# Kernel tuning notes

Measured on AMD Instinct MI355X. Metric: run time of the kernel, lower is better.

Reference implementation:

```python
import jax, jax.numpy as jnp
import numpy as np

N = 100000      # nodes
E = 3200000     # edges
NG = 64         # graphs in batch
F_IN, H1, H2 = 128, 128, 64
DENSE = 16 * 8  # first_dense_neurons * second_dense_neurons
LABELS = 2


def setup_inputs() -> dict:
    key = jax.random.key(0)
    ks = jax.random.split(key, 12)
    x = jax.random.normal(ks[0], (N, F_IN), dtype=jnp.float32)
    edge_index = jax.random.randint(ks[1], (2, E), 0, N, dtype=jnp.int32)
    batch = jnp.sort(jax.random.randint(ks[2], (N,), 0, NG, dtype=jnp.int32))
    s = 0.05
    W1 = jax.random.normal(ks[3], (F_IN, H1), dtype=jnp.float32) * s
    b1 = jnp.zeros((H1,), dtype=jnp.float32)
    W2 = jax.random.normal(ks[4], (H1, H2), dtype=jnp.float32) * s
    b2 = jnp.zeros((H2,), dtype=jnp.float32)
    Wf1 = jax.random.normal(ks[5], (H2, DENSE), dtype=jnp.float32) * s
    bf1 = jnp.zeros((DENSE,), dtype=jnp.float32)
    Wf2 = jax.random.normal(ks[6], (DENSE, LABELS), dtype=jnp.float32) * s
    bf2 = jnp.zeros((LABELS,), dtype=jnp.float32)
    return {"x": x, "W1": W1, "b1": b1, "W2": W2, "b2": b2,
            "Wf1": Wf1, "bf1": bf1, "Wf2": Wf2, "bf2": bf2,
            "edge_index": edge_index, "batch": batch}


def _gcn_conv(x, W, b, src, dst, dis):
    # PyG GCNConv: h = x @ W, propagate with sym norm (self-loops included)
    h = x @ W
    coef = (dis[src] * dis[dst])[:, None]          # [E,1]
    agg = jax.ops.segment_sum(h[src] * coef, dst, num_segments=N)
    agg = agg + h * (dis * dis)[:, None]           # self-loop term
    return agg + b


def reference(x, W1, b1, W2, b2, Wf1, bf1, Wf2, bf2, edge_index, batch):
    src, dst = edge_index[0], edge_index[1]
    # degree with self-loops, symmetric normalization D^-1/2 (A+I) D^-1/2
    deg = 1.0 + jax.ops.segment_sum(jnp.ones((E,), x.dtype), dst, num_segments=N)
    dis = jax.lax.rsqrt(deg)
    h1 = jax.nn.relu(_gcn_conv(x, W1, b1, src, dst, dis))
    h2 = jax.nn.relu(_gcn_conv(h1, W2, b2, src, dst, dis))
    a1 = h2 @ Wf1 + bf1                            # [N, DENSE] (dropout: eval mode)
    counts = jax.ops.segment_sum(jnp.ones((N,), x.dtype), batch, num_segments=NG)
    graph_embedding = jax.ops.segment_sum(a1, batch, num_segments=NG) / jnp.maximum(counts, 1.0)[:, None]
    ic_predictions = graph_embedding @ Wf2 + bf2   # [NG, LABELS]
    penalty = jnp.float32(0.0)
    return (graph_embedding, penalty, ic_predictions)
```

## Files before the change

### kernel.cpp

```cpp
#include <hip/hip_runtime.h>


typedef __attribute__((ext_vector_type(8))) short bfrag;
typedef __attribute__((ext_vector_type(16))) float f32x16;
typedef __attribute__((ext_vector_type(2))) float floatx2;

__device__ __forceinline__ unsigned short f2bf(float f) {
    unsigned int u = __builtin_bit_cast(unsigned int, f);
    u = (u + 0x7FFFu + ((u >> 16) & 1u)) >> 16;
    return (unsigned short)u;
}
__device__ __forceinline__ float bf2f(unsigned int lo16) {
    unsigned int v = lo16 << 16;
    return __builtin_bit_cast(float, v);
}
__device__ __forceinline__ unsigned char f2fp8(float f) {
    return (unsigned char)(__builtin_amdgcn_cvt_pk_fp8_f32(f, f, 0, false) & 0xFF);
}
__device__ __forceinline__ void macc8f8(float* acc, const uint2& v, float c) {
    floatx2 f0 = __builtin_amdgcn_cvt_pk_f32_fp8((int)v.x, false);
    floatx2 f1 = __builtin_amdgcn_cvt_pk_f32_fp8((int)v.x, true);
    floatx2 f2 = __builtin_amdgcn_cvt_pk_f32_fp8((int)v.y, false);
    floatx2 f3 = __builtin_amdgcn_cvt_pk_f32_fp8((int)v.y, true);
    acc[0] += f0.x * c; acc[1] += f0.y * c;
    acc[2] += f1.x * c; acc[3] += f1.y * c;
    acc[4] += f2.x * c; acc[5] += f2.y * c;
    acc[6] += f3.x * c; acc[7] += f3.y * c;
}

template <int K, int NC>
__device__ __forceinline__ void wprep_body(int bid, const float* __restrict__ W,
                                           unsigned short* __restrict__ Wf) {
    constexpr int CT = NC / 32, KT = K / 16;
    int idx = bid * 256 + threadIdx.x;
    if (idx >= KT * CT * 64) return;
    int l = idx & 63;
    int fi = idx >> 6;
    int ct = fi % CT, kt = fi / CT;
    int n = ct * 32 + (l & 31);
    int k0 = kt * 16 + 8 * (l >> 5);
    unsigned short v[8];
#pragma unroll
    for (int j = 0; j < 8; ++j) v[j] = f2bf(W[(size_t)(k0 + j) * NC + n]);
    uint4 o;
    o.x = (unsigned)v[0] | ((unsigned)v[1] << 16);
    o.y = (unsigned)v[2] | ((unsigned)v[3] << 16);
    o.z = (unsigned)v[4] | ((unsigned)v[5] << 16);
    o.w = (unsigned)v[6] | ((unsigned)v[7] << 16);
    *(uint4*)&Wf[(size_t)idx * 8] = o;
}

__global__ __launch_bounds__(256) void fusedA_kernel(const int* __restrict__ dst,
                                                     int* __restrict__ bcount, int E, int EB,
                                                     const float* __restrict__ W1,
                                                     unsigned short* __restrict__ Wp1,
                                                     const float* __restrict__ W2,
                                                     unsigned short* __restrict__ Wp2) {
    __shared__ int h[256];
    int b = blockIdx.x;
    int t = threadIdx.x;
    if (b < EB) {
        h[t] = 0;
        __syncthreads();
        int base = b * 4096;
#pragma unroll
        for (int i = 0; i < 16; ++i) {
            int e = base + t + i * 256;
            if (e < E) atomicAdd(&h[dst[e] >> 9], 1);
        }
        __syncthreads();
        if (h[t] > 0) atomicAdd(&bcount[t], h[t]);
    } else if (b < EB + 8) {
        wprep_body<128, 128>(b - EB, W1, Wp1);
    } else {
        wprep_body<128, 64>(b - EB - 8, W2, Wp2);
    }
}

__global__ __launch_bounds__(256) void bucket_scatter_kernel(const int* __restrict__ src,
                                                             const int* __restrict__ dst,
                                                             const int* __restrict__ bcount,
                                                             int* __restrict__ bfill,
                                                             unsigned int* __restrict__ stage,
                                                             int E) {
    __shared__ int sc[256];
    __shared__ int hist[256];
    __shared__ int abase[256];
    int t = threadIdx.x;
    int bc = bcount[t];
    sc[t] = bc;
    __syncthreads();
    for (int off = 1; off < 256; off <<= 1) {
        int tmp = 0;
        if (t >= off) tmp = sc[t - off];
        __syncthreads();
        sc[t] += tmp;
        __syncthreads();
    }
    int bstart_t = sc[t] - bc;
    hist[t] = 0;
    __syncthreads();
    int base = blockIdx.x * 4096;
#pragma unroll
    for (int i = 0; i < 16; ++i) {
        int e = base + t + i * 256;
        if (e < E) atomicAdd(&hist[dst[e] >> 9], 1);
    }
    __syncthreads();
    if (hist[t] > 0) {
        int r = atomicAdd(&bfill[t], hist[t]);
        abase[t] = bstart_t + r;
    }
    __syncthreads();
    hist[t] = 0;
    __syncthreads();
#pragma unroll
    for (int i = 0; i < 16; ++i) {
        int e = base + t + i * 256;
        if (e < E) {
            int d = dst[e];
            int b = d >> 9;
            int slot = atomicAdd(&hist[b], 1);
            stage[abase[b] + slot] = (unsigned)src[e] | ((unsigned)(d & 511) << 17);
        }
    }
}

__global__ __launch_bounds__(256) void csr_build_kernel(const unsigned int* __restrict__ stage,
                                                        const int* __restrict__ bcount,
                                                        int* __restrict__ rowstart,
                                                        float* __restrict__ dis,
                                                        int* __restrict__ csr_src,
                                                        int N, int NB, int E) {
    __shared__ int sc[256];
    __shared__ int cnt[512];
    __shared__ int ofs[512];
    __shared__ int psum[256];
    int b = blockIdx.x, t = threadIdx.x;
    int bc = bcount[t];
    sc[t] = bc;
    __syncthreads();
    for (int off = 1; off < 256; off <<= 1) {
        int tmp = 0;
        if (t >= off) tmp = sc[t - off];
        __syncthreads();
        sc[t] += tmp;
        __syncthreads();
    }
    int ee = sc[b];
    int eb = ee - bcount[b];
    if (b == NB - 1 && t == 0) rowstart[N] = E;
    int node0 = b << 9;
    int nb = min(512, N - node0);
    cnt[t] = 0;
    cnt[t + 256] = 0;
    __syncthreads();
    for (int e = eb + t; e < ee; e += 256) {
        unsigned w = stage[e];
        atomicAdd(&cnt[w >> 17], 1);
    }
    __syncthreads();
    int a = cnt[2 * t], c = cnt[2 * t + 1];
    int ps = a + c;
    psum[t] = ps;
    __syncthreads();
    for (int off = 1; off < 256; off <<= 1) {
        int tmp = 0;
        if (t >= off) tmp = psum[t - off];
        __syncthreads();
        psum[t] += tmp;
        __syncthreads();
    }
    int ex = psum[t] - ps;
    ofs[2 * t] = ex;
    ofs[2 * t + 1] = ex + a;
    if (2 * t < nb) {
        rowstart[node0 + 2 * t] = eb + ex;
        dis[node0 + 2 * t] = rsqrtf(1.f + (float)a);
    }
    if (2 * t + 1 < nb) {
        rowstart[node0 + 2 * t + 1] = eb + ex + a;
        dis[node0 + 2 * t + 1] = rsqrtf(1.f + (float)c);
    }
    __syncthreads();
    for (int e = eb + t; e < ee; e += 256) {
        unsigned w = stage[e];
        int l = w >> 17;
        int slot = atomicAdd(&ofs[l], 1);
        csr_src[eb + slot] = (int)(w & 0x1FFFFu);
    }
}

template <int K, int NC, bool IN_F32>
__global__ __launch_bounds__(256) void gemm_mfma_kernel(const void* __restrict__ Av,
                                                        const unsigned short* __restrict__ Wf,
                                                        unsigned char* __restrict__ C,
                                                        int M) {
    constexpr int KT = K / 16, CT = NC / 32;
    int wid = (blockIdx.x * blockDim.x + threadIdx.x) >> 6;
    int lane = threadIdx.x & 63;
    int row0 = wid * 32;
    if (row0 >= M) return;

    bfrag B[KT][CT];
#pragma unroll
    for (int kt = 0; kt < KT; ++kt)
#pragma unroll
        for (int ct = 0; ct < CT; ++ct)
            B[kt][ct] = *(const bfrag*)&Wf[(size_t)((kt * CT + ct) * 64 + lane) * 8];

    f32x16 acc[CT];
#pragma unroll
    for (int ct = 0; ct < CT; ++ct)
#pragma unroll
        for (int i = 0; i < 16; ++i) acc[ct][i] = 0.f;

    int r = row0 + (lane & 31);
    if (r >= M) r = M - 1;
#pragma unroll
    for (int kt = 0; kt < KT; ++kt) {
        bfrag a;
        if (IN_F32) {
            const float* Arow = &((const float*)Av)[(size_t)r * K + 8 * (lane >> 5)];
            float4 v0 = *(const float4*)&Arow[kt * 16];
            float4 v1 = *(const float4*)&Arow[kt * 16 + 4];
            a[0] = (short)f2bf(v0.x); a[1] = (short)f2bf(v0.y);
            a[2] = (short)f2bf(v0.z); a[3] = (short)f2bf(v0.w);
            a[4] = (short)f2bf(v1.x); a[5] = (short)f2bf(v1.y);
            a[6] = (short)f2bf(v1.z); a[7] = (short)f2bf(v1.w);
        } else {
            const unsigned short* Arow =
                &((const unsigned short*)Av)[(size_t)r * K + 8 * (lane >> 5)];
            a = *(const bfrag*)&Arow[kt * 16];
        }
#pragma unroll
        for (int ct = 0; ct < CT; ++ct)
            acc[ct] = __builtin_amdgcn_mfma_f32_32x32x16_bf16(a, B[kt][ct], acc[ct], 0, 0, 0);
    }

    int colb = lane & 31;
    int rowq = 4 * (lane >> 5);
#pragma unroll
    for (int ct = 0; ct < CT; ++ct) {
        int col = ct * 32 + colb;
#pragma unroll
        for (int rg = 0; rg < 16; ++rg) {
            int row = row0 + (rg & 3) + 8 * (rg >> 2) + rowq;
            if (row < M) C[(size_t)row * NC + col] = f2fp8(acc[ct][rg]);
        }
    }
}

template <int NC>
__global__ __launch_bounds__(256) void aggregate_kernel(const unsigned char* __restrict__ h,
                                                        const float* __restrict__ dis,
                                                        const int* __restrict__ rowstart,
                                                        const int* __restrict__ csr_src,
                                                        const float* __restrict__ bias,
                                                        unsigned short* __restrict__ out,
                                                        int N) {
    constexpr int LPR = NC / 8;
    constexpr int RPS = 64 / LPR;
    int wid = (blockIdx.x * blockDim.x + threadIdx.x) >> 6;
    int lane = threadIdx.x & 63;
    if (wid >= N) return;
    int n = wid;
    int sub = lane / LPR;
    int fid = lane % LPR;
    const uint2* h8 = (const uint2*)h;
    float d = dis[n];
    float acc[8];
#pragma unroll
    for (int i = 0; i < 8; ++i) acc[i] = 0.f;
    if (sub == 0) {
        uint2 hv = h8[(size_t)n * LPR + fid];
        macc8f8(acc, hv, d);
    }

    int beg = rowstart[n], end = rowstart[n + 1];
    for (int e0 = beg; e0 < end; e0 += 64) {
        int idx = e0 + lane;
        int sv = 0;
        float dv = 0.f;
        if (idx < end) {
            sv = __builtin_nontemporal_load(&csr_src[idx]);
            dv = dis[sv];
        }
        int cnt = min(64, end - e0);
        int j = 0;
        for (; j + 4 * RPS <= cnt; j += 4 * RPS) {
            int ja = j + sub, jb = j + RPS + sub, jc2 = j + 2 * RPS + sub,
                jd = j + 3 * RPS + sub;
            int sa = __shfl(sv, ja); float ca = __shfl(dv, ja);
            int sb = __shfl(sv, jb); float cb = __shfl(dv, jb);
            int sc = __shfl(sv, jc2); float cc = __shfl(dv, jc2);
            int sd = __shfl(sv, jd); float cd = __shfl(dv, jd);
            uint2 va = h8[(size_t)sa * LPR + fid];
            uint2 vb = h8[(size_t)sb * LPR + fid];
            uint2 vc = h8[(size_t)sc * LPR + fid];
            uint2 vd = h8[(size_t)sd * LPR + fid];
            macc8f8(acc, va, ca);
            macc8f8(acc, vb, cb);
            macc8f8(acc, vc, cc);
            macc8f8(acc, vd, cd);
        }
        for (; j + 2 * RPS <= cnt; j += 2 * RPS) {
            int ja = j + sub, jb = j + RPS + sub;
            int sa = __shfl(sv, ja); float ca = __shfl(dv, ja);
            int sb = __shfl(sv, jb); float cb = __shfl(dv, jb);
            uint2 va = h8[(size_t)sa * LPR + fid];
            uint2 vb = h8[(size_t)sb * LPR + fid];
            macc8f8(acc, va, ca);
            macc8f8(acc, vb, cb);
        }
        for (; j < cnt; j += RPS) {
            int jj = j + sub;
            int jc = min(jj, cnt - 1);
            int s = __shfl(sv, jc);
            float c = __shfl(dv, jc);
            if (jj >= cnt) c = 0.f;
            uint2 v = h8[(size_t)s * LPR + fid];
            macc8f8(acc, v, c);
        }
    }
#pragma unroll
    for (int m = LPR; m < 64; m <<= 1) {
#pragma unroll
        for (int i = 0; i < 8; ++i) acc[i] += __shfl_xor(acc[i], m);
    }
    if (sub == 0) {
        const float4 bv0 = *(const float4*)&bias[fid * 8 + 0];
        const float4 bv1 = *(const float4*)&bias[fid * 8 + 4];
        float r[8];
        r[0] = fmaxf(acc[0] * d + bv0.x, 0.f);
        r[1] = fmaxf(acc[1] * d + bv0.y, 0.f);
        r[2] = fmaxf(acc[2] * d + bv0.z, 0.f);
        r[3] = fmaxf(acc[3] * d + bv0.w, 0.f);
        r[4] = fmaxf(acc[4] * d + bv1.x, 0.f);
        r[5] = fmaxf(acc[5] * d + bv1.y, 0.f);
        r[6] = fmaxf(acc[6] * d + bv1.z, 0.f);
        r[7] = fmaxf(acc[7] * d + bv1.w, 0.f);
        uint4 o;
        o.x = (unsigned)f2bf(r[0]) | ((unsigned)f2bf(r[1]) << 16);
        o.y = (unsigned)f2bf(r[2]) | ((unsigned)f2bf(r[3]) << 16);
        o.z = (unsigned)f2bf(r[4]) | ((unsigned)f2bf(r[5]) << 16);
        o.w = (unsigned)f2bf(r[6]) | ((unsigned)f2bf(r[7]) << 16);
        *(uint4*)&out[(size_t)n * NC + fid * 8] = o;
    }
}

__global__ __launch_bounds__(256) void poolcount_kernel(const unsigned short* __restrict__ h2,
                                                        const int* __restrict__ batch,
                                                        float* __restrict__ gsum,
                                                        int* __restrict__ gcnt,
                                                        int N, int PB) {
    int t = threadIdx.x;
    if ((int)blockIdx.x < PB) {
        int fid = t & 63;
        int strip = t >> 6;
        int n0 = blockIdx.x * 128;
        int nend = min(n0 + 128, N);
        int n = n0 + strip;
        if (n < nend) {
            float acc = 0.f;
            int gcur = batch[n];
            for (; n < nend; n += 4) {
                int g = batch[n];
                if (g != gcur) {
                    atomicAdd(&gsum[gcur * 64 + fid], acc);
                    acc = 0.f;
                    gcur = g;
                }
                acc += bf2f(h2[(size_t)n * 64 + fid]);
            }
            atomicAdd(&gsum[gcur * 64 + fid], acc);
        }
    } else {
        __shared__ int lc[64];
        if (t < 64) lc[t] = 0;
        __syncthreads();
        int n = ((int)blockIdx.x - PB) * 256 + t;
        if (n < N) atomicAdd(&lc[batch[n]], 1);
        __syncthreads();
        if (t < 64 && lc[t] > 0) atomicAdd(&gcnt[t], lc[t]);
    }
}

__global__ __launch_bounds__(128) void head_kernel(const float* __restrict__ gsum,
                                                   const int* __restrict__ gcnt,
                                                   const float* __restrict__ Wf1,
                                                   const float* __restrict__ bf1,
                                                   const float* __restrict__ Wf2,
                                                   const float* __restrict__ bf2,
                                                   float* __restrict__ out) {
    __shared__ float ph[64];
    __shared__ float red0[128], red1[128];
    int g = blockIdx.x, f = threadIdx.x;
    if (f < 64) ph[f] = gsum[g * 64 + f] / (float)max(gcnt[g], 1);
    __syncthreads();
    float ge = bf1[f];
#pragma unroll 8
    for (int k = 0; k < 64; ++k) ge += ph[k] * Wf1[k * 128 + f];
    out[g * 128 + f] = ge;
    red0[f] = ge * Wf2[f * 2 + 0];
    red1[f] = ge * Wf2[f * 2 + 1];
    __syncthreads();
    for (int off = 64; off > 0; off >>= 1) {
        if (f < off) { red0[f] += red0[f + off]; red1[f] += red1[f + off]; }
        __syncthreads();
    }
    if (f == 0) {
        out[8192 + 1 + g * 2 + 0] = red0[0] + bf2[0];
        out[8192 + 1 + g * 2 + 1] = red1[0] + bf2[1];
        if (g == 0) out[8192] = 0.f;
    }
}

extern "C" void kernel_launch(void* const* d_in, const int* in_sizes, int n_in,
                              void* d_out, int out_size, void* d_ws, size_t ws_size,
                              hipStream_t stream) {
    const float* x   = (const float*)d_in[0];
    const float* W1  = (const float*)d_in[1];
    const float* b1  = (const float*)d_in[2];
    const float* W2  = (const float*)d_in[3];
    const float* b2  = (const float*)d_in[4];
    const float* Wf1 = (const float*)d_in[5];
    const float* bf1 = (const float*)d_in[6];
    const float* Wf2 = (const float*)d_in[7];
    const float* bf2 = (const float*)d_in[8];
    const int* edge  = (const int*)d_in[9];
    const int* batch = (const int*)d_in[10];

    const int N = in_sizes[10];
    const int E = in_sizes[9] / 2;
    const int* srcA = edge;
    const int* dstA = edge + E;
    float* out = (float*)d_out;

    const int NB = (N + 511) >> 9;

    char* p = (char*)d_ws;
    auto alloc = [&](size_t bytes) {
        char* r = p;
        p += (bytes + 255) & ~(size_t)255;
        return r;
    };
    float* gsum     = (float*)alloc(64 * 64 * 4);
    int*   gcnt     = (int*)alloc(64 * 4);
    int*   bcount   = (int*)alloc(256 * 4);
    int*   bfill    = (int*)alloc(256 * 4);
    size_t zbytes   = (size_t)(p - (char*)d_ws);
    float* dis      = (float*)alloc((size_t)N * 4);
    int*   rowstart = (int*)alloc((size_t)(N + 1) * 4);
    unsigned short* Wp1 = (unsigned short*)alloc(8 * 4 * 64 * 8 * 2);
    unsigned short* Wp2 = (unsigned short*)alloc(8 * 2 * 64 * 8 * 2);
    unsigned int* stage = (unsigned int*)alloc((size_t)E * 4);
    int*   csr_src  = (int*)alloc((size_t)E * 4);
    unsigned char*  hf8   = (unsigned char*)alloc((size_t)N * 128);
    unsigned short* h1b   = (unsigned short*)alloc((size_t)N * 128 * 2);
    unsigned short* h2b   = (unsigned short*)alloc((size_t)N * 64 * 2);

    (void)hipMemsetAsync(d_ws, 0, zbytes, stream);

    const int EB = (E + 4095) / 4096;
    fusedA_kernel<<<EB + 12, 256, 0, stream>>>(dstA, bcount, E, EB, W1, Wp1, W2, Wp2);
    bucket_scatter_kernel<<<EB, 256, 0, stream>>>(srcA, dstA, bcount, bfill, stage, E);
    csr_build_kernel<<<NB, 256, 0, stream>>>(stage, bcount, rowstart, dis, csr_src,
                                             N, NB, E);

    const int GB = (N + 127) / 128;
    gemm_mfma_kernel<128, 128, true><<<GB, 256, 0, stream>>>(x, Wp1, hf8, N);
    aggregate_kernel<128><<<(N + 3) / 4, 256, 0, stream>>>(hf8, dis, rowstart, csr_src,
                                                           b1, h1b, N);
    gemm_mfma_kernel<128, 64, false><<<GB, 256, 0, stream>>>(h1b, Wp2, hf8, N);
    aggregate_kernel<64><<<(N + 3) / 4, 256, 0, stream>>>(hf8, dis, rowstart, csr_src,
                                                          b2, h2b, N);
    const int PB = (N + 127) / 128;
    const int CB = (N + 255) / 256;
    poolcount_kernel<<<PB + CB, 256, 0, stream>>>(h2b, batch, gsum, gcnt, N, PB);
    head_kernel<<<64, 128, 0, stream>>>(gsum, gcnt, Wf1, bf1, Wf2, bf2, out);
}
```

Before: 406.2 us.

## Merge CSR build with first GEMM launch and cache edges in registers/LDS

Runs the CSR build blocks and the first-layer MFMA GEMM blocks in one launch, so the two independent stages overlap and one launch is removed. The CSR build now stages each bucket's edge words in a ~56KB shared array so the second pass reads LDS instead of reloading from global memory. The bucket scatter keeps dst values in registers between its two passes instead of reading them twice. The large shared allocation now applies to GEMM blocks as well, which lowers occupancy for the fused kernel.

```diff
diff --git a/kernel.cpp b/kernel.cpp
--- a/kernel.cpp
+++ b/kernel.cpp
@@ -101,10 +101,12 @@
     hist[t] = 0;
     __syncthreads();
     int base = blockIdx.x * 4096;
+    int dcache[16];
 #pragma unroll
     for (int i = 0; i < 16; ++i) {
         int e = base + t + i * 256;
-        if (e < E) atomicAdd(&hist[dst[e] >> 9], 1);
+        dcache[i] = (e < E) ? dst[e] : -1;
+        if (dcache[i] >= 0) atomicAdd(&hist[dcache[i] >> 9], 1);
     }
     __syncthreads();
     if (hist[t] > 0) {
@@ -117,8 +119,8 @@
 #pragma unroll
     for (int i = 0; i < 16; ++i) {
         int e = base + t + i * 256;
-        if (e < E) {
-            int d = dst[e];
+        int d = dcache[i];
+        if (d >= 0) {
             int b = d >> 9;
             int slot = atomicAdd(&hist[b], 1);
             stage[abase[b] + slot] = (unsigned)src[e] | ((unsigned)(d & 511) << 17);
@@ -126,17 +128,19 @@
     }
 }
 
-__global__ __launch_bounds__(256) void csr_build_kernel(const unsigned int* __restrict__ stage,
-                                                        const int* __restrict__ bcount,
-                                                        int* __restrict__ rowstart,
-                                                        float* __restrict__ dis,
-                                                        int* __restrict__ csr_src,
-                                                        int N, int NB, int E) {
+#define SCAP 14336
+__device__ __forceinline__ void csr_build_body(int b, const unsigned int* __restrict__ stage,
+                                               const int* __restrict__ bcount,
+                                               int* __restrict__ rowstart,
+                                               float* __restrict__ dis,
+                                               int* __restrict__ csr_src,
+                                               int N, int NB, int E) {
     __shared__ int sc[256];
     __shared__ int cnt[512];
     __shared__ int ofs[512];
     __shared__ int psum[256];
-    int b = blockIdx.x, t = threadIdx.x;
+    __shared__ unsigned int sedge[SCAP];
+    int t = threadIdx.x;
     int bc = bcount[t];
     sc[t] = bc;
     __syncthreads();
@@ -157,6 +161,8 @@
     __syncthreads();
     for (int e = eb + t; e < ee; e += 256) {
         unsigned w = stage[e];
+        int le = e - eb;
+        if (le < SCAP) sedge[le] = w;
         atomicAdd(&cnt[w >> 17], 1);
     }
     __syncthreads();
@@ -184,7 +190,8 @@
     }
     __syncthreads();
     for (int e = eb + t; e < ee; e += 256) {
-        unsigned w = stage[e];
+        int le = e - eb;
+        unsigned w = (le < SCAP) ? sedge[le] : stage[e];
         int l = w >> 17;
         int slot = atomicAdd(&ofs[l], 1);
         csr_src[eb + slot] = (int)(w & 0x1FFFFu);
@@ -192,12 +199,11 @@
 }
 
 template <int K, int NC, bool IN_F32>
-__global__ __launch_bounds__(256) void gemm_mfma_kernel(const void* __restrict__ Av,
-                                                        const unsigned short* __restrict__ Wf,
-                                                        unsigned char* __restrict__ C,
-                                                        int M) {
+__device__ __forceinline__ void gemm_body(int gb, const void* __restrict__ Av,
+                                          const unsigned short* __restrict__ Wf,
+                                          unsigned char* __restrict__ C, int M) {
     constexpr int KT = K / 16, CT = NC / 32;
-    int wid = (blockIdx.x * blockDim.x + threadIdx.x) >> 6;
+    int wid = gb * 4 + (int)(threadIdx.x >> 6);
     int lane = threadIdx.x & 63;
     int row0 = wid * 32;
     if (row0 >= M) return;
@@ -249,6 +255,31 @@
             if (row < M) C[(size_t)row * NC + col] = f2fp8(acc[ct][rg]);
         }
     }
+}
+
+__global__ __launch_bounds__(256) void fusedB_kernel(const unsigned int* __restrict__ stage,
+                                                     const int* __restrict__ bcount,
+                                                     int* __restrict__ rowstart,
+                                                     float* __restrict__ dis,
+                                                     int* __restrict__ csr_src,
+                                                     int N, int NB, int E,
+                                                     const float* __restrict__ x,
+                                                     const unsigned short* __restrict__ Wp1,
+                                                     unsigned char* __restrict__ hf8) {
+    int b = blockIdx.x;
+    if (b < NB) {
+        csr_build_body(b, stage, bcount, rowstart, dis, csr_src, N, NB, E);
+    } else {
+        gemm_body<128, 128, true>(b - NB, x, Wp1, hf8, N);
+    }
+}
+
+template <int K, int NC, bool IN_F32>
+__global__ __launch_bounds__(256) void gemm_mfma_kernel(const void* __restrict__ Av,
+                                                        const unsigned short* __restrict__ Wf,
+                                                        unsigned char* __restrict__ C,
+                                                        int M) {
+    gemm_body<K, NC, IN_F32>(blockIdx.x, Av, Wf, C, M);
 }
 
 template <int NC>
@@ -463,13 +494,11 @@
     (void)hipMemsetAsync(d_ws, 0, zbytes, stream);
 
     const int EB = (E + 4095) / 4096;
+    const int GB = (N + 127) / 128;
     fusedA_kernel<<<EB + 12, 256, 0, stream>>>(dstA, bcount, E, EB, W1, Wp1, W2, Wp2);
     bucket_scatter_kernel<<<EB, 256, 0, stream>>>(srcA, dstA, bcount, bfill, stage, E);
-    csr_build_kernel<<<NB, 256, 0, stream>>>(stage, bcount, rowstart, dis, csr_src,
-                                             N, NB, E);
-
-    const int GB = (N + 127) / 128;
-    gemm_mfma_kernel<128, 128, true><<<GB, 256, 0, stream>>>(x, Wp1, hf8, N);
+    fusedB_kernel<<<NB + GB, 256, 0, stream>>>(stage, bcount, rowstart, dis, csr_src,
+                                               N, NB, E, x, Wp1, hf8);
     aggregate_kernel<128><<<(N + 3) / 4, 256, 0, stream>>>(hf8, dis, rowstart, csr_src,
                                                            b1, h1b, N);
     gemm_mfma_kernel<128, 64, false><<<GB, 256, 0, stream>>>(h1b, Wp2, hf8, N);
```

Measured after the change: 380.1 us (median of 2 runs). 6.4% less time.
